# Kernel optimization log

Measured on AMD Instinct MI355X. Metric: run time of the kernel, lower is better.

## Reference

```python
import jax, jax.numpy as jnp
import numpy as np

VOCAB, E, H, POL = 50000, 512, 512, 3
B, T, TA = 128, 256, 8
D = H + E  # attention embed dim (hidden_dim + embed_dim)


def setup_inputs() -> dict:
    key = jax.random.key(0)
    ks = jax.random.split(key, 12)
    s = lambda k, shape, f: jax.random.normal(k, shape, jnp.float32) * f
    return {
        # indices drawn in [1, VOCAB) so 0 remains the padding id (here all tokens valid)
        "text_indices": jax.random.randint(ks[0], (B, T), 1, VOCAB),
        "aspect_indices": jax.random.randint(ks[1], (B, TA), 1, VOCAB),
        "embed_table": s(ks[2], (VOCAB, E), 0.1),
        "w_ih": s(ks[3], (2 * E, 3 * H), 0.02),   # sampled Bayesian GRU input weights
        "w_hh": s(ks[4], (H, 3 * H), 0.02),       # sampled Bayesian GRU hidden weights
        "b_gru": jnp.zeros((3 * H,), jnp.float32),
        "wk_w": s(ks[5], (D, D), 0.02),
        "wk_b": jnp.zeros((D,), jnp.float32),
        "wq_w": s(ks[6], (D, D), 0.02),
        "wq_b": jnp.zeros((D,), jnp.float32),
        "q_param": s(ks[7], (1, D), 0.05),         # NoQueryAttention learned query
        "bil_w": s(ks[8], (D, D), 0.02),           # bi_linear score weight
        "dense_w": s(ks[9], (H, POL), 0.02),
        "dense_b": jnp.zeros((POL,), jnp.float32),
    }


def _gru(x, w_ih, w_hh, b):
    # x: (B, T, I) -> hidden sequence (B, T, H); standard GRU recurrence with
    # given (per-forward sampled) weights, matching blitz BayesianGRU math.
    Hs = w_hh.shape[0]
    xg = jnp.einsum('bti,ij->btj', x, w_ih) + b  # precompute input gates once: (B,T,3H)

    def step(h, xg_t):
        hg = h @ w_hh  # (B, 3H)
        r = jax.nn.sigmoid(xg_t[:, :Hs] + hg[:, :Hs])
        z = jax.nn.sigmoid(xg_t[:, Hs:2 * Hs] + hg[:, Hs:2 * Hs])
        n = jnp.tanh(xg_t[:, 2 * Hs:] + r * hg[:, 2 * Hs:])
        h = (1.0 - z) * n + z * h
        return h, h

    h0 = jnp.zeros((x.shape[0], Hs), x.dtype)
    _, hs = jax.lax.scan(step, h0, jnp.swapaxes(xg, 0, 1))  # (T, B, H)
    return jnp.swapaxes(hs, 0, 1)


def reference(text_indices, aspect_indices, embed_table, w_ih, w_hh, b_gru,
              wk_w, wk_b, wq_w, wq_b, q_param, bil_w, dense_w, dense_b):
    mask = (text_indices != 0).astype(jnp.float32)              # (B, T)
    x = embed_table[text_indices] * mask[..., None]              # SqueezeEmbedding zeros padding
    asp = embed_table[aspect_indices]                            # (B, TA, E)
    a_len = (aspect_indices != 0).sum(-1).astype(jnp.float32)    # (B,)
    asp_pool = asp.sum(1) / a_len[:, None]                       # (B, E)
    aspect = jnp.broadcast_to(asp_pool[:, None, :], (x.shape[0], x.shape[1], asp_pool.shape[-1]))
    xin = jnp.concatenate([aspect, x], axis=-1)                  # (B, T, 2E)

    h = _gru(xin, w_ih, w_hh, b_gru)                             # (B, T, H)

    # NoQueryAttention (bi_linear score, n_head=1); only the score is used downstream.
    ha = jnp.concatenate([h, aspect], axis=-1)                   # (B, T, D)
    kx = ha @ wk_w + wk_b                                        # (B, T, D)
    qx = q_param @ wq_w + wq_b                                   # (1, D)
    qw = qx @ bil_w                                              # (1, D)
    score = jax.nn.softmax(jnp.einsum('qd,btd->bt', qw, kx), axis=-1)  # (B, T)
    pooled = jnp.einsum('bt,bth->bh', score, h)                  # (B, H)
    return pooled @ dense_w + dense_b                            # (B, POL)
```

## Files before the change

kernel.cpp:

```cpp
#include <hip/hip_runtime.h>
#include <hip/hip_bf16.h>

#define B_ 128
#define T_ 256
#define TA_ 8
#define E_ 512
#define H_ 512
#define D_ 1024
#define G3_ 1536
#define TC_ 16
#define NCH_ 16

typedef __attribute__((ext_vector_type(8))) short bf16x8_;
typedef __attribute__((ext_vector_type(4))) float f32x4_;

__device__ __forceinline__ float sigmoidf_(float x) { return 1.0f / (1.0f + __expf(-x)); }

__device__ __forceinline__ unsigned short f2bf_(float f) {
  unsigned u = __float_as_uint(f);
  return (unsigned short)((u + 0x7FFFu + ((u >> 16) & 1u)) >> 16);
}
__device__ __forceinline__ float bf2f_(unsigned short b) {
  return __uint_as_float((unsigned)b << 16);
}

__global__ __launch_bounds__(256) void k_transpose(const float* __restrict__ w, float* __restrict__ wt) {
  __shared__ float tile[32][33];
  const int tx = threadIdx.x & 31, ty = threadIdx.x >> 5;
  const int c0 = blockIdx.x * 32, i0 = blockIdx.y * 32;
#pragma unroll
  for (int r = 0; r < 4; ++r) {
    int ii = ty + r * 8;
    tile[ii][tx] = w[(size_t)(i0 + ii) * G3_ + c0 + tx];
  }
  __syncthreads();
#pragma unroll
  for (int r = 0; r < 4; ++r) {
    int cc = ty + r * 8;
    wt[(size_t)(c0 + cc) * H_ + i0 + tx] = tile[tx][cc];
  }
}

__global__ __launch_bounds__(256) void k_prep_bsplit(const float* __restrict__ w_ih,
                                                     unsigned short* __restrict__ Bhg,
                                                     unsigned short* __restrict__ Blg) {
  __shared__ float tile[32][33];
  const int tx = threadIdx.x & 31, ty = threadIdx.x >> 5;
  const int g0 = blockIdx.x * 32, kk0 = blockIdx.y * 32;
#pragma unroll
  for (int r = 0; r < 4; ++r) {
    int kl = ty + r * 8;
    tile[kl][tx] = w_ih[(size_t)(E_ + kk0 + kl) * G3_ + g0 + tx];
  }
  __syncthreads();
#pragma unroll
  for (int r = 0; r < 4; ++r) {
    const int gl = ty + r * 8;
    const float f = tile[tx][gl];
    const unsigned short hb = f2bf_(f);
    Bhg[(size_t)(g0 + gl) * E_ + kk0 + tx] = hb;
    Blg[(size_t)(g0 + gl) * E_ + kk0 + tx] = f2bf_(f - bf2f_(hb));
  }
}

__global__ __launch_bounds__(256) void k_asp_pool(const int* __restrict__ aidx, const float* __restrict__ embed,
                                                  float* __restrict__ ap) {
  const int b = blockIdx.x;
  int ai[TA_]; int cnt = 0;
#pragma unroll
  for (int ta = 0; ta < TA_; ++ta) { ai[ta] = aidx[b * TA_ + ta]; cnt += (ai[ta] != 0); }
  const float inv = 1.0f / (float)cnt;
  for (int e = threadIdx.x; e < E_; e += 256) {
    float s = 0.f;
#pragma unroll
    for (int ta = 0; ta < TA_; ++ta) s += embed[(size_t)ai[ta] * E_ + e];
    ap[b * E_ + e] = s * inv;
  }
}

__global__ __launch_bounds__(256) void k_matvecT(const float* __restrict__ v, const float* __restrict__ W,
                                                 const float* __restrict__ bias, float* __restrict__ y,
                                                 int J, int N) {
  __shared__ float v_s[1024];
  for (int i = threadIdx.x; i < J; i += 256) v_s[i] = v[i];
  __syncthreads();
  const int d = blockIdx.x * 256 + threadIdx.x;
  float acc = bias ? bias[d] : 0.f;
  for (int j = 0; j < J; j += 4) {
    acc += v_s[j + 0] * W[(size_t)(j + 0) * N + d];
    acc += v_s[j + 1] * W[(size_t)(j + 1) * N + d];
    acc += v_s[j + 2] * W[(size_t)(j + 2) * N + d];
    acc += v_s[j + 3] * W[(size_t)(j + 3) * N + d];
  }
  y[d] = acc;
}

__global__ __launch_bounds__(256) void k_u(const float* __restrict__ wk, const float* __restrict__ qw,
                                           float* __restrict__ u) {
  __shared__ float q_s[D_];
  for (int i = threadIdx.x; i < D_; i += 256) q_s[i] = qw[i];
  __syncthreads();
  const int lane = threadIdx.x & 63, wave = threadIdx.x >> 6;
  const int k = blockIdx.x * 4 + wave;
  float p = 0.f;
#pragma unroll
  for (int m = 0; m < 16; ++m) { int d = lane + m * 64; p += wk[(size_t)k * D_ + d] * q_s[d]; }
#pragma unroll
  for (int off = 32; off > 0; off >>= 1) p += __shfl_down(p, off);
  if (lane == 0) u[k] = p;
}

__global__ __launch_bounds__(256) void k_ag(const float* __restrict__ ap, const float* __restrict__ w_ih,
                                            const float* __restrict__ bg, float* __restrict__ ag) {
  __shared__ float a_s[4][E_];
  const int g0 = blockIdx.x * 256, b0 = blockIdx.y * 4;
#pragma unroll
  for (int r = 0; r < 2; ++r) {
    int li = threadIdx.x + r * 256;
    int row = li >> 7, c4 = (li & 127) * 4;
    *(float4*)&a_s[row][c4] = *(const float4*)&ap[(size_t)(b0 + row) * E_ + c4];
  }
  __syncthreads();
  const int g = g0 + threadIdx.x;
  float acc0 = 0.f, acc1 = 0.f, acc2 = 0.f, acc3 = 0.f;
  for (int i4 = 0; i4 < 128; ++i4) {
    const float* wp = &w_ih[(size_t)(i4 * 4) * G3_ + g];
    float w0 = wp[0], w1 = wp[G3_], w2 = wp[2 * G3_], w3 = wp[3 * G3_];
    float4 a0 = *(const float4*)&a_s[0][i4 * 4];
    float4 a1 = *(const float4*)&a_s[1][i4 * 4];
    float4 a2 = *(const float4*)&a_s[2][i4 * 4];
    float4 a3 = *(const float4*)&a_s[3][i4 * 4];
    acc0 += a0.x * w0 + a0.y * w1 + a0.z * w2 + a0.w * w3;
    acc1 += a1.x * w0 + a1.y * w1 + a1.z * w2 + a1.w * w3;
    acc2 += a2.x * w0 + a2.y * w1 + a2.z * w2 + a2.w * w3;
    acc3 += a3.x * w0 + a3.y * w1 + a3.z * w2 + a3.w * w3;
  }
  const float bgv = bg[g];
  ag[(size_t)(b0 + 0) * G3_ + g] = acc0 + bgv;
  ag[(size_t)(b0 + 1) * G3_ + g] = acc1 + bgv;
  ag[(size_t)(b0 + 2) * G3_ + g] = acc2 + bgv;
  ag[(size_t)(b0 + 3) * G3_ + g] = acc3 + bgv;
}

__global__ __launch_bounds__(256) void k_gemm_xg_mfma(const int* __restrict__ tidx,
                                                      const float* __restrict__ embed,
                                                      const unsigned short* __restrict__ Bhg,
                                                      const unsigned short* __restrict__ Blg,
                                                      const float* __restrict__ ag,
                                                      float* __restrict__ xg, int chunk) {
  __shared__ __align__(16) unsigned short Ah[64][40], Al[64][40];
  __shared__ __align__(16) unsigned short Bh[64][40], Bl[64][40];
  const int tid = threadIdx.x;
  const int g0 = blockIdx.x * 64, m0 = blockIdx.y * 64;
  const int lane = tid & 63, wv = tid >> 6;
  const int wr = wv >> 1, wc = wv & 1;
  const int lr = lane & 15, lk8 = (lane >> 4) * 8;

  const int arow = tid >> 2, ak8 = (tid & 3) * 8;
  const int am = m0 + arow;
  const int ab = am >> 4;
  const int at = chunk * TC_ + (am & 15);
  const int tix = tidx[ab * T_ + at];
  const float* aptr = embed + (size_t)tix * E_ + ak8;
  const float amask = (tix != 0) ? 1.f : 0.f;

  const int bcol = tid >> 2, bk8 = (tid & 3) * 8;
  const unsigned short* bph = Bhg + (size_t)(g0 + bcol) * E_ + bk8;
  const unsigned short* bpl = Blg + (size_t)(g0 + bcol) * E_ + bk8;

  f32x4_ acc[2][2] = {{{0.f,0.f,0.f,0.f},{0.f,0.f,0.f,0.f}},
                      {{0.f,0.f,0.f,0.f},{0.f,0.f,0.f,0.f}}};

  for (int k0 = 0; k0 < E_; k0 += 32) {
    {
      float fv[8];
      *(float4*)&fv[0] = *(const float4*)(aptr + k0);
      *(float4*)&fv[4] = *(const float4*)(aptr + k0 + 4);
      bf16x8_ h8, l8;
#pragma unroll
      for (int j = 0; j < 8; ++j) {
        const float f = fv[j] * amask;
        const unsigned short hb = f2bf_(f);
        h8[j] = (short)hb;
        l8[j] = (short)f2bf_(f - bf2f_(hb));
      }
      *(bf16x8_*)&Ah[arow][ak8] = h8;
      *(bf16x8_*)&Al[arow][ak8] = l8;
    }
    *(bf16x8_*)&Bh[bcol][bk8] = *(const bf16x8_*)(bph + k0);
    *(bf16x8_*)&Bl[bcol][bk8] = *(const bf16x8_*)(bpl + k0);
    __syncthreads();

    bf16x8_ a_hi[2], a_lo[2], b_hi[2], b_lo[2];
#pragma unroll
    for (int s = 0; s < 2; ++s) {
      a_hi[s] = *(const bf16x8_*)&Ah[wr * 32 + s * 16 + lr][lk8];
      a_lo[s] = *(const bf16x8_*)&Al[wr * 32 + s * 16 + lr][lk8];
      b_hi[s] = *(const bf16x8_*)&Bh[wc * 32 + s * 16 + lr][lk8];
      b_lo[s] = *(const bf16x8_*)&Bl[wc * 32 + s * 16 + lr][lk8];
    }
#pragma unroll
    for (int sr = 0; sr < 2; ++sr)
#pragma unroll
      for (int sc = 0; sc < 2; ++sc) {
        acc[sr][sc] = __builtin_amdgcn_mfma_f32_16x16x32_bf16(a_hi[sr], b_hi[sc], acc[sr][sc], 0, 0, 0);
        acc[sr][sc] = __builtin_amdgcn_mfma_f32_16x16x32_bf16(a_hi[sr], b_lo[sc], acc[sr][sc], 0, 0, 0);
        acc[sr][sc] = __builtin_amdgcn_mfma_f32_16x16x32_bf16(a_lo[sr], b_hi[sc], acc[sr][sc], 0, 0, 0);
      }
    __syncthreads();
  }

#pragma unroll
  for (int sr = 0; sr < 2; ++sr)
#pragma unroll
    for (int sc = 0; sc < 2; ++sc)
#pragma unroll
      for (int r = 0; r < 4; ++r) {
        const int m = m0 + wr * 32 + sr * 16 + (lane >> 4) * 4 + r;
        const int g = g0 + wc * 32 + sc * 16 + lr;
        const int b = m >> 4;
        xg[(size_t)m * G3_ + g] = acc[sr][sc][r] + ag[(size_t)b * G3_ + g];
      }
}

__global__ __launch_bounds__(512, 2) void k_gru_chunk(const float* __restrict__ whhT,
                                                      const float* __restrict__ xg,
                                                      unsigned long long* __restrict__ hA,
                                                      unsigned long long* __restrict__ hB,
                                                      float* __restrict__ hs,
                                                      int chunk) {
  __shared__ __align__(16) unsigned short h_hi_s[16 * 520];
  __shared__ __align__(16) unsigned short h_lo_s[16 * 520];
  __shared__ float hexact_s[16][16];
  __shared__ __align__(16) float cbuf_s[3][64][4];
  __shared__ float csum_s[3][16][17];

  const int tid = threadIdx.x;
  const int kg = blockIdx.x >> 3;
  const int bg = blockIdx.x & 7;
  const int k0 = kg * 16, b0 = bg * 16;
  const int lane = tid & 63, wv = tid >> 6;
  const int gate = wv >> 1, kseg = wv & 1;
  const int lrow = lane & 15, lhi = lane >> 4;
  const int gb = tid >> 4, tx = tid & 15;

  bf16x8_ bhi[8], blo[8];
  if (wv < 6) {
    const float* wp = &whhT[((size_t)(gate * H_ + k0 + lrow)) * H_ + kseg * 256 + lhi * 8];
#pragma unroll
    for (int ks = 0; ks < 8; ++ks) {
      float fv[8];
      *(float4*)&fv[0] = *(const float4*)(wp + ks * 32);
      *(float4*)&fv[4] = *(const float4*)(wp + ks * 32 + 4);
      bf16x8_ h8, l8;
#pragma unroll
      for (int j = 0; j < 8; ++j) {
        const unsigned short hb = f2bf_(fv[j]);
        h8[j] = (short)hb;
        l8[j] = (short)f2bf_(fv[j] - bf2f_(hb));
      }
      bhi[ks] = h8; blo[ks] = l8;
    }
  }

  for (int tc = 0; tc < TC_; ++tc) {
    const int t = chunk * TC_ + tc;
    const unsigned long long* hsrc = (t & 1) ? hB : hA;
    unsigned long long*       hdst = (t & 1) ? hA : hB;
    const unsigned tagc = (unsigned)t;

    float xr = 0.f, xz = 0.f, xn = 0.f;
    if (tid < 256) {
      const float* xrow = xg + ((size_t)(b0 + gb) * TC_ + tc) * G3_;
      const int k = k0 + tx;
      xr = xrow[k]; xz = xrow[H_ + k]; xn = xrow[2 * H_ + k];
    }

#pragma unroll
    for (int half = 0; half < 2; ++half) {
      unsigned long long v[8];
#pragma unroll
      for (int ii = 0; ii < 8; ++ii)
        v[ii] = __hip_atomic_load(&hsrc[(size_t)(b0 + half * 8 + ii) * H_ + tid],
                                  __ATOMIC_RELAXED, __HIP_MEMORY_SCOPE_AGENT);
      unsigned pend = 0xFFu;
      while (pend) {
#pragma unroll
        for (int ii = 0; ii < 8; ++ii) {
          if ((pend >> ii) & 1u) {
            if ((unsigned)(v[ii] >> 32) == tagc) {
              union { unsigned u; float f; } cv;
              cv.u = (unsigned)(v[ii] & 0xFFFFFFFFull);
              const int r = half * 8 + ii;
              const unsigned short hb = f2bf_(cv.f);
              h_hi_s[r * 520 + tid] = hb;
              h_lo_s[r * 520 + tid] = f2bf_(cv.f - bf2f_(hb));
              if ((unsigned)(tid - k0) < 16u) hexact_s[r][tid - k0] = cv.f;
              pend &= ~(1u << ii);
            } else {
              v[ii] = __hip_atomic_load(&hsrc[(size_t)(b0 + half * 8 + ii) * H_ + tid],
                                        __ATOMIC_RELAXED, __HIP_MEMORY_SCOPE_AGENT);
            }
          }
        }
        if (pend) __builtin_amdgcn_s_sleep(1);
      }
    }
    __syncthreads();

    f32x4_ c = {0.f, 0.f, 0.f, 0.f};
    if (wv < 6) {
      const int abase = lrow * 520 + kseg * 256 + lhi * 8;
#pragma unroll
      for (int ks = 0; ks < 8; ++ks) {
        const bf16x8_ ahi = *(const bf16x8_*)&h_hi_s[abase + ks * 32];
        const bf16x8_ alo = *(const bf16x8_*)&h_lo_s[abase + ks * 32];
        c = __builtin_amdgcn_mfma_f32_16x16x32_bf16(ahi, bhi[ks], c, 0, 0, 0);
        c = __builtin_amdgcn_mfma_f32_16x16x32_bf16(ahi, blo[ks], c, 0, 0, 0);
        c = __builtin_amdgcn_mfma_f32_16x16x32_bf16(alo, bhi[ks], c, 0, 0, 0);
      }
      if (kseg == 1) *(f32x4_*)&cbuf_s[gate][lane][0] = c;
    }
    __syncthreads();

    if (wv < 6 && kseg == 0) {
      const f32x4_ c2 = *(const f32x4_*)&cbuf_s[gate][lane][0];
#pragma unroll
      for (int r = 0; r < 4; ++r)
        csum_s[gate][lhi * 4 + r][lrow] = c[r] + c2[r];
    }
    __syncthreads();

    if (tid < 256) {
      const float sR = csum_s[0][gb][tx];
      const float sZ = csum_s[1][gb][tx];
      const float sN = csum_s[2][gb][tx];
      const float hp = hexact_s[gb][tx];
      const float gr = sigmoidf_(xr + sR);
      const float gz = sigmoidf_(xz + sZ);
      const float gn = tanhf(xn + gr * sN);
      const float hv = (1.f - gz) * gn + gz * hp;
      const int k = k0 + tx;
      union { float f; unsigned u; } cv; cv.f = hv;
      __hip_atomic_store(&hdst[(size_t)(b0 + gb) * H_ + k],
                         ((unsigned long long)(unsigned)(t + 1) << 32) | (unsigned long long)cv.u,
                         __ATOMIC_RELAXED, __HIP_MEMORY_SCOPE_AGENT);
      hs[((size_t)(b0 + gb) * T_ + t) * H_ + k] = hv;
    }
  }
}

__global__ __launch_bounds__(256) void k_logits(const float* __restrict__ hs, const float* __restrict__ u,
                                                float* __restrict__ lg) {
  __shared__ float u_s[H_];
  for (int i = threadIdx.x; i < H_; i += 256) u_s[i] = u[i];
  __syncthreads();
  const int lane = threadIdx.x & 63, wave = threadIdx.x >> 6;
  const int wid = blockIdx.x * 4 + wave;
  const float* hrow = hs + (size_t)wid * H_;
  float p = 0.f;
#pragma unroll
  for (int m = 0; m < 8; ++m) { int d = lane + m * 64; p += hrow[d] * u_s[d]; }
#pragma unroll
  for (int off = 32; off > 0; off >>= 1) p += __shfl_down(p, off);
  if (lane == 0) lg[wid] = p;
}

__global__ __launch_bounds__(256) void k_softmax_pool(const float* __restrict__ lg, const float* __restrict__ hs,
                                                      float* __restrict__ pooled) {
  __shared__ float sw[256];
  __shared__ float red[8];
  const int b = blockIdx.x, tid = threadIdx.x;
  const int lane = tid & 63, wave = tid >> 6;
  const float lv = lg[b * T_ + tid];
  float mx = lv;
#pragma unroll
  for (int off = 32; off > 0; off >>= 1) mx = fmaxf(mx, __shfl_down(mx, off));
  if (lane == 0) red[wave] = mx;
  __syncthreads();
  if (tid == 0) red[4] = fmaxf(fmaxf(red[0], red[1]), fmaxf(red[2], red[3]));
  __syncthreads();
  mx = red[4];
  const float p = __expf(lv - mx);
  float sm = p;
#pragma unroll
  for (int off = 32; off > 0; off >>= 1) sm += __shfl_down(sm, off);
  if (lane == 0) red[wave] = sm;
  __syncthreads();
  if (tid == 0) red[5] = red[0] + red[1] + red[2] + red[3];
  __syncthreads();
  sw[tid] = p / red[5];
  __syncthreads();
  float a0 = 0.f, a1 = 0.f;
  const float* hbase = hs + (size_t)b * T_ * H_;
  for (int t = 0; t < T_; ++t) {
    const float s = sw[t];
    a0 += s * hbase[(size_t)t * H_ + tid];
    a1 += s * hbase[(size_t)t * H_ + 256 + tid];
  }
  pooled[b * H_ + tid] = a0;
  pooled[b * H_ + 256 + tid] = a1;
}

__global__ __launch_bounds__(64) void k_dense(const float* __restrict__ pooled, const float* __restrict__ dw,
                                              const float* __restrict__ db, float* __restrict__ out) {
  const int b = blockIdx.x, lane = threadIdx.x;
  float a0 = 0.f, a1 = 0.f, a2 = 0.f;
#pragma unroll
  for (int m = 0; m < 8; ++m) {
    int h = lane + m * 64;
    float pv = pooled[b * H_ + h];
    a0 += pv * dw[h * 3 + 0];
    a1 += pv * dw[h * 3 + 1];
    a2 += pv * dw[h * 3 + 2];
  }
#pragma unroll
  for (int off = 32; off > 0; off >>= 1) {
    a0 += __shfl_down(a0, off);
    a1 += __shfl_down(a1, off);
    a2 += __shfl_down(a2, off);
  }
  if (lane == 0) {
    out[b * 3 + 0] = a0 + db[0];
    out[b * 3 + 1] = a1 + db[1];
    out[b * 3 + 2] = a2 + db[2];
  }
}

extern "C" void kernel_launch(void* const* d_in, const int* in_sizes, int n_in,
                              void* d_out, int out_size, void* d_ws, size_t ws_size,
                              hipStream_t stream) {
  (void)in_sizes; (void)n_in; (void)out_size; (void)ws_size;
  const int*   tidx  = (const int*)d_in[0];
  const int*   aidx  = (const int*)d_in[1];
  const float* embed = (const float*)d_in[2];
  const float* w_ih  = (const float*)d_in[3];
  const float* w_hh  = (const float*)d_in[4];
  const float* b_gru = (const float*)d_in[5];
  const float* wk_w  = (const float*)d_in[6];
  const float* wq_w  = (const float*)d_in[8];
  const float* wq_b  = (const float*)d_in[9];
  const float* q_p   = (const float*)d_in[10];
  const float* bil_w = (const float*)d_in[11];
  const float* dw    = (const float*)d_in[12];
  const float* db    = (const float*)d_in[13];
  float* out = (float*)d_out;

  float* ws = (float*)d_ws;
  size_t off = 0;
  unsigned long long* hA64 = (unsigned long long*)(ws + off); off += (size_t)B_ * H_ * 2;
  unsigned long long* hB64 = (unsigned long long*)(ws + off); off += (size_t)B_ * H_ * 2;
  unsigned short* Bhg = (unsigned short*)(ws + off); off += (size_t)G3_ * E_ / 2;
  unsigned short* Blg = (unsigned short*)(ws + off); off += (size_t)G3_ * E_ / 2;
  float* ap     = ws + off; off += (size_t)B_ * E_;
  float* ag     = ws + off; off += (size_t)B_ * G3_;
  float* qx     = ws + off; off += D_;
  float* qw     = ws + off; off += D_;
  float* u      = ws + off; off += H_;
  float* lg     = ws + off; off += (size_t)B_ * T_;
  float* pooled = ws + off; off += (size_t)B_ * H_;
  float* whhT   = ws + off; off += (size_t)G3_ * H_;
  float* xgbuf  = ws + off; off += (size_t)B_ * TC_ * G3_;
  float* hs     = ws + off; off += (size_t)B_ * T_ * H_;

  hipMemsetAsync(hA64, 0, (size_t)B_ * H_ * 2 * sizeof(unsigned long long), stream);

  k_transpose<<<dim3(48, 16), 256, 0, stream>>>(w_hh, whhT);
  k_prep_bsplit<<<dim3(48, 16), 256, 0, stream>>>(w_ih, Bhg, Blg);
  k_asp_pool<<<B_, 256, 0, stream>>>(aidx, embed, ap);
  k_matvecT<<<4, 256, 0, stream>>>(q_p, wq_w, wq_b, qx, D_, D_);
  k_matvecT<<<4, 256, 0, stream>>>(qx, bil_w, nullptr, qw, D_, D_);
  k_u<<<128, 256, 0, stream>>>(wk_w, qw, u);
  k_ag<<<dim3(6, 32), 256, 0, stream>>>(ap, w_ih, b_gru, ag);

  for (int chunk = 0; chunk < NCH_; ++chunk) {
    k_gemm_xg_mfma<<<dim3(24, 32), 256, 0, stream>>>(tidx, embed, Bhg, Blg, ag, xgbuf, chunk);
    int ch = chunk;
    void* args[] = { (void*)&whhT, (void*)&xgbuf, (void*)&hA64, (void*)&hB64,
                     (void*)&hs, (void*)&ch };
    hipLaunchCooperativeKernel((const void*)k_gru_chunk, dim3(256), dim3(512),
                               args, 0, stream);
  }

  k_logits<<<8192, 256, 0, stream>>>(hs, u, lg);
  k_softmax_pool<<<B_, 256, 0, stream>>>(lg, hs, pooled);
  k_dense<<<B_, 64, 0, stream>>>(pooled, dw, db, out);
}
```

Measured before the change: 2.437 ms.

## Enlarge GRU time chunks to 64 steps and drop a per-step barrier

Makes the time-chunk size a runtime parameter and raises it from 16 to 64 steps when the workspace is large enough, which cuts the number of xg GEMM and cooperative GRU launches from 16 to 4. The GRU step kernel now has both k-segment waves write their MFMA partials to shared memory and lets the elementwise threads sum them directly. This removes the intermediate csum buffer and one __syncthreads per step. The larger chunk needs a bigger xg workspace buffer and falls back to 16 steps if that does not fit.

```diff
diff --git a/kernel.cpp b/kernel.cpp
--- a/kernel.cpp
+++ b/kernel.cpp
@@ -8,8 +8,6 @@
 #define H_ 512
 #define D_ 1024
 #define G3_ 1536
-#define TC_ 16
-#define NCH_ 16
 
 typedef __attribute__((ext_vector_type(8))) short bf16x8_;
 typedef __attribute__((ext_vector_type(4))) float f32x4_;
@@ -147,7 +145,8 @@
                                                       const unsigned short* __restrict__ Bhg,
                                                       const unsigned short* __restrict__ Blg,
                                                       const float* __restrict__ ag,
-                                                      float* __restrict__ xg, int chunk) {
+                                                      float* __restrict__ xg,
+                                                      int sc, int tsc, int tshift) {
   __shared__ __align__(16) unsigned short Ah[64][40], Al[64][40];
   __shared__ __align__(16) unsigned short Bh[64][40], Bl[64][40];
   const int tid = threadIdx.x;
@@ -158,8 +157,8 @@
 
   const int arow = tid >> 2, ak8 = (tid & 3) * 8;
   const int am = m0 + arow;
-  const int ab = am >> 4;
-  const int at = chunk * TC_ + (am & 15);
+  const int ab = am >> tshift;
+  const int at = sc * tsc + (am & (tsc - 1));
   const int tix = tidx[ab * T_ + at];
   const float* aptr = embed + (size_t)tix * E_ + ak8;
   const float amask = (tix != 0) ? 1.f : 0.f;
@@ -202,10 +201,10 @@
 #pragma unroll
     for (int sr = 0; sr < 2; ++sr)
 #pragma unroll
-      for (int sc = 0; sc < 2; ++sc) {
-        acc[sr][sc] = __builtin_amdgcn_mfma_f32_16x16x32_bf16(a_hi[sr], b_hi[sc], acc[sr][sc], 0, 0, 0);
-        acc[sr][sc] = __builtin_amdgcn_mfma_f32_16x16x32_bf16(a_hi[sr], b_lo[sc], acc[sr][sc], 0, 0, 0);
-        acc[sr][sc] = __builtin_amdgcn_mfma_f32_16x16x32_bf16(a_lo[sr], b_hi[sc], acc[sr][sc], 0, 0, 0);
+      for (int sc2 = 0; sc2 < 2; ++sc2) {
+        acc[sr][sc2] = __builtin_amdgcn_mfma_f32_16x16x32_bf16(a_hi[sr], b_hi[sc2], acc[sr][sc2], 0, 0, 0);
+        acc[sr][sc2] = __builtin_amdgcn_mfma_f32_16x16x32_bf16(a_hi[sr], b_lo[sc2], acc[sr][sc2], 0, 0, 0);
+        acc[sr][sc2] = __builtin_amdgcn_mfma_f32_16x16x32_bf16(a_lo[sr], b_hi[sc2], acc[sr][sc2], 0, 0, 0);
       }
     __syncthreads();
   }
@@ -213,13 +212,13 @@
 #pragma unroll
   for (int sr = 0; sr < 2; ++sr)
 #pragma unroll
-    for (int sc = 0; sc < 2; ++sc)
+    for (int sc2 = 0; sc2 < 2; ++sc2)
 #pragma unroll
       for (int r = 0; r < 4; ++r) {
         const int m = m0 + wr * 32 + sr * 16 + (lane >> 4) * 4 + r;
-        const int g = g0 + wc * 32 + sc * 16 + lr;
-        const int b = m >> 4;
-        xg[(size_t)m * G3_ + g] = acc[sr][sc][r] + ag[(size_t)b * G3_ + g];
+        const int g = g0 + wc * 32 + sc2 * 16 + lr;
+        const int b = m >> tshift;
+        xg[(size_t)m * G3_ + g] = acc[sr][sc2][r] + ag[(size_t)b * G3_ + g];
       }
 }
 
@@ -228,12 +227,11 @@
                                                       unsigned long long* __restrict__ hA,
                                                       unsigned long long* __restrict__ hB,
                                                       float* __restrict__ hs,
-                                                      int chunk) {
+                                                      int sc, int tsc) {
   __shared__ __align__(16) unsigned short h_hi_s[16 * 520];
   __shared__ __align__(16) unsigned short h_lo_s[16 * 520];
   __shared__ float hexact_s[16][16];
-  __shared__ __align__(16) float cbuf_s[3][64][4];
-  __shared__ float csum_s[3][16][17];
+  __shared__ __align__(16) float cbuf_s[3][2][64][4];
 
   const int tid = threadIdx.x;
   const int kg = blockIdx.x >> 3;
@@ -263,15 +261,15 @@
     }
   }
 
-  for (int tc = 0; tc < TC_; ++tc) {
-    const int t = chunk * TC_ + tc;
+  for (int tcc = 0; tcc < tsc; ++tcc) {
+    const int t = sc * tsc + tcc;
     const unsigned long long* hsrc = (t & 1) ? hB : hA;
     unsigned long long*       hdst = (t & 1) ? hA : hB;
     const unsigned tagc = (unsigned)t;
 
     float xr = 0.f, xz = 0.f, xn = 0.f;
     if (tid < 256) {
-      const float* xrow = xg + ((size_t)(b0 + gb) * TC_ + tc) * G3_;
+      const float* xrow = xg + ((size_t)(b0 + gb) * tsc + tcc) * G3_;
       const int k = k0 + tx;
       xr = xrow[k]; xz = xrow[H_ + k]; xn = xrow[2 * H_ + k];
     }
@@ -308,8 +306,8 @@
     }
     __syncthreads();
 
-    f32x4_ c = {0.f, 0.f, 0.f, 0.f};
     if (wv < 6) {
+      f32x4_ c = {0.f, 0.f, 0.f, 0.f};
       const int abase = lrow * 520 + kseg * 256 + lhi * 8;
 #pragma unroll
       for (int ks = 0; ks < 8; ++ks) {
@@ -319,31 +317,25 @@
         c = __builtin_amdgcn_mfma_f32_16x16x32_bf16(ahi, blo[ks], c, 0, 0, 0);
         c = __builtin_amdgcn_mfma_f32_16x16x32_bf16(alo, bhi[ks], c, 0, 0, 0);
       }
-      if (kseg == 1) *(f32x4_*)&cbuf_s[gate][lane][0] = c;
+      *(f32x4_*)&cbuf_s[gate][kseg][lane][0] = c;
     }
     __syncthreads();
 
-    if (wv < 6 && kseg == 0) {
-      const f32x4_ c2 = *(const f32x4_*)&cbuf_s[gate][lane][0];
-#pragma unroll
-      for (int r = 0; r < 4; ++r)
-        csum_s[gate][lhi * 4 + r][lrow] = c[r] + c2[r];
-    }
-    __syncthreads();
-
     if (tid < 256) {
-      const float sR = csum_s[0][gb][tx];
-      const float sZ = csum_s[1][gb][tx];
-      const float sN = csum_s[2][gb][tx];
+      const int lane2 = ((gb >> 2) << 4) | tx;
+      const int reg = gb & 3;
+      const float sR = cbuf_s[0][0][lane2][reg] + cbuf_s[0][1][lane2][reg];
+      const float sZ = cbuf_s[1][0][lane2][reg] + cbuf_s[1][1][lane2][reg];
+      const float sN = cbuf_s[2][0][lane2][reg] + cbuf_s[2][1][lane2][reg];
       const float hp = hexact_s[gb][tx];
       const float gr = sigmoidf_(xr + sR);
       const float gz = sigmoidf_(xz + sZ);
       const float gn = tanhf(xn + gr * sN);
       const float hv = (1.f - gz) * gn + gz * hp;
       const int k = k0 + tx;
-      union { float f; unsigned u; } cv; cv.f = hv;
       __hip_atomic_store(&hdst[(size_t)(b0 + gb) * H_ + k],
-                         ((unsigned long long)(unsigned)(t + 1) << 32) | (unsigned long long)cv.u,
+                         ((unsigned long long)(unsigned)(t + 1) << 32) |
+                             (unsigned long long)__float_as_uint(hv),
                          __ATOMIC_RELAXED, __HIP_MEMORY_SCOPE_AGENT);
       hs[((size_t)(b0 + gb) * T_ + t) * H_ + k] = hv;
     }
@@ -430,7 +422,7 @@
 extern "C" void kernel_launch(void* const* d_in, const int* in_sizes, int n_in,
                               void* d_out, int out_size, void* d_ws, size_t ws_size,
                               hipStream_t stream) {
-  (void)in_sizes; (void)n_in; (void)out_size; (void)ws_size;
+  (void)in_sizes; (void)n_in; (void)out_size;
   const int*   tidx  = (const int*)d_in[0];
   const int*   aidx  = (const int*)d_in[1];
   const float* embed = (const float*)d_in[2];
@@ -446,6 +438,16 @@
   const float* db    = (const float*)d_in[13];
   float* out = (float*)d_out;
 
+  const size_t fixed_floats =
+      (size_t)B_ * H_ * 2 * 2 +
+      (size_t)G3_ * E_ / 2 * 2 +
+      (size_t)B_ * E_ + (size_t)B_ * G3_ + D_ + D_ + H_ +
+      (size_t)B_ * T_ + (size_t)B_ * H_ +
+      (size_t)G3_ * H_ + (size_t)B_ * T_ * H_;
+  int TSC = 64, TSHIFT = 6;
+  if ((fixed_floats + (size_t)B_ * 64 * G3_) * 4 > ws_size) { TSC = 16; TSHIFT = 4; }
+  const int NSC = T_ / TSC;
+
   float* ws = (float*)d_ws;
   size_t off = 0;
   unsigned long long* hA64 = (unsigned long long*)(ws + off); off += (size_t)B_ * H_ * 2;
@@ -460,7 +462,7 @@
   float* lg     = ws + off; off += (size_t)B_ * T_;
   float* pooled = ws + off; off += (size_t)B_ * H_;
   float* whhT   = ws + off; off += (size_t)G3_ * H_;
-  float* xgbuf  = ws + off; off += (size_t)B_ * TC_ * G3_;
+  float* xgbuf  = ws + off; off += (size_t)B_ * TSC * G3_;
   float* hs     = ws + off; off += (size_t)B_ * T_ * H_;
 
   hipMemsetAsync(hA64, 0, (size_t)B_ * H_ * 2 * sizeof(unsigned long long), stream);
@@ -473,11 +475,12 @@
   k_u<<<128, 256, 0, stream>>>(wk_w, qw, u);
   k_ag<<<dim3(6, 32), 256, 0, stream>>>(ap, w_ih, b_gru, ag);
 
-  for (int chunk = 0; chunk < NCH_; ++chunk) {
-    k_gemm_xg_mfma<<<dim3(24, 32), 256, 0, stream>>>(tidx, embed, Bhg, Blg, ag, xgbuf, chunk);
-    int ch = chunk;
+  for (int sc = 0; sc < NSC; ++sc) {
+    k_gemm_xg_mfma<<<dim3(24, B_ * TSC / 64), 256, 0, stream>>>(
+        tidx, embed, Bhg, Blg, ag, xgbuf, sc, TSC, TSHIFT);
+    int scA = sc, tscA = TSC;
     void* args[] = { (void*)&whhT, (void*)&xgbuf, (void*)&hA64, (void*)&hB64,
-                     (void*)&hs, (void*)&ch };
+                     (void*)&hs, (void*)&scA, (void*)&tscA };
     hipLaunchCooperativeKernel((const void*)k_gru_chunk, dim3(256), dim3(512),
                                args, 0, stream);
   }
```

Result: faster. 2.020 ms, median of 2 (-17.1%).
